# Performance work log

Measured on AMD Instinct MI355X. Metric: run time of the kernel, lower is better.

## Reference

```python
import jax, jax.numpy as jnp
import numpy as np

B, L, E, H = 2, 2048, 1024, 16
HD = E // H


def _rel_shift(x):
    # x: [b, h, q, k] -> Transformer-XL relative shift via pad+reshape trick
    b, h, q, k = x.shape
    xp = jnp.pad(x, ((0, 0), (0, 0), (0, 0), (1, 0)))  # pad left of last dim
    xp = xp.reshape(b, h, k + 1, q)
    return xp[:, :, 1:, :].reshape(b, h, q, k)


def setup_inputs() -> dict:
    key = jax.random.key(0)
    ks = jax.random.split(key, 16)
    s = 0.02
    return {
        "query": jax.random.normal(ks[0], (B, L, E), jnp.float32),
        "key": jax.random.normal(ks[1], (B, L, E), jnp.float32),
        "value": jax.random.normal(ks[2], (B, L, E), jnp.float32),
        "pos_embedding": jax.random.normal(ks[3], (B, L, E), jnp.float32),
        "Wq": jax.random.normal(ks[4], (E, E), jnp.float32) * s,
        "bq": jnp.zeros((E,), jnp.float32),
        "Wk": jax.random.normal(ks[5], (E, E), jnp.float32) * s,
        "bk": jnp.zeros((E,), jnp.float32),
        "Wv": jax.random.normal(ks[6], (E, E), jnp.float32) * s,
        "bv": jnp.zeros((E,), jnp.float32),
        "Wp": jax.random.normal(ks[7], (E, E), jnp.float32) * s,  # Pos linear, no bias
        "Wo": jax.random.normal(ks[8], (E, E), jnp.float32) * s,
        "bo": jnp.zeros((E,), jnp.float32),
        "U": jax.random.normal(ks[9], (H, HD), jnp.float32) * s,
        "V": jax.random.normal(ks[10], (H, HD), jnp.float32) * s,
    }


def reference(query, key, value, pos_embedding, Wq, bq, Wk, bk, Wv, bv, Wp, Wo, bo, U, V):
    b, qlen, e = query.shape
    h, hd = U.shape
    scale = jnp.sqrt(jnp.asarray(e, query.dtype))
    # torch Linear: y = x @ W.T + b
    q = (query @ Wq.T + bq).reshape(b, qlen, h, hd)
    k = (key @ Wk.T + bk).reshape(b, key.shape[1], h, hd)
    v = (value @ Wv.T + bv).reshape(b, value.shape[1], h, hd)
    r = (pos_embedding @ Wp.T).reshape(b, -1, h, hd)
    content_score = jnp.einsum("bqhd,bkhd->bhqk", q + U, k)
    position_score = jnp.einsum("bqhd,bkhd->bhqk", q + V, r)
    position_score = _rel_shift(position_score)
    attention_score = (content_score + position_score) / scale
    # NOTE: the original module applies NO softmax; faithful reproduction.
    # einsum 'bhqk,bvhd->bqhd' sums over both k (scores) and v (values).
    alpha = jnp.einsum("bhqk,bvhd->bqhd", attention_score, v).reshape(b, qlen, e)
    return alpha @ Wo.T + bo
```

## Files before the change

kernel.cpp:

```cpp
#include <hip/hip_runtime.h>

#define BB 2
#define LL 2048
#define EE 1024
#define HH 16
#define HDD 64

typedef __bf16 bf16x8 __attribute__((ext_vector_type(8)));
typedef float f32x4 __attribute__((ext_vector_type(4)));

__device__ __forceinline__ unsigned short f2bf(float f) {
  unsigned int x = __float_as_uint(f);
  return (unsigned short)((x + 0x7FFFu + ((x >> 16) & 1u)) >> 16);
}

__device__ __forceinline__ void load_lds16(const void* g, void* l) {
  __builtin_amdgcn_global_load_lds(
      (const __attribute__((address_space(1))) void*)g,
      (__attribute__((address_space(3))) void*)l, 16, 0, 0);
}

#define CAST_BLOCKS 1280
#define CAST_STRIDE (CAST_BLOCKS * 256)
__global__ __launch_bounds__(256) void prelude_kernel(
    const float* __restrict__ q, const float* __restrict__ pe,
    const float* __restrict__ wq, const float* __restrict__ wp,
    unsigned short* __restrict__ q16, unsigned short* __restrict__ pe16,
    unsigned short* __restrict__ wq16, unsigned short* __restrict__ wp16,
    const float* __restrict__ key, const float* __restrict__ value,
    float* __restrict__ keysum, float* __restrict__ valsum) {
  if (blockIdx.x < CAST_BLOCKS) {
    const int NQ4 = BB * LL * EE / 4;
    const int NW4 = EE * EE / 4;
    int t = blockIdx.x * 256 + threadIdx.x;
    float4 v[8]; unsigned short* dst[8]; int off[8];
#pragma unroll
    for (int k = 0; k < 8; k++) {
      int i = t + k * CAST_STRIDE;
      const float* src;
      if (i < NQ4)                { src = q;  dst[k] = q16;  off[k] = i; }
      else if (i < 2 * NQ4)       { src = pe; dst[k] = pe16; off[k] = i - NQ4; }
      else if (i < 2 * NQ4 + NW4) { src = wq; dst[k] = wq16; off[k] = i - 2 * NQ4; }
      else                        { src = wp; dst[k] = wp16; off[k] = i - 2 * NQ4 - NW4; }
      v[k] = ((const float4*)src)[off[k]];
    }
#pragma unroll
    for (int k = 0; k < 8; k++) {
      ushort4 u;
      u.x = f2bf(v[k].x); u.y = f2bf(v[k].y); u.z = f2bf(v[k].z); u.w = f2bf(v[k].w);
      ((ushort4*)dst[k])[off[k]] = u;
    }
  } else {
    int blk2 = blockIdx.x - CAST_BLOCKS;
    int b = blk2 >> 6, ch = blk2 & 63;
    int tid = threadIdx.x;
    const float4* k4 = (const float4*)(key   + ((size_t)b * LL + ch * 32) * EE);
    const float4* v4 = (const float4*)(value + ((size_t)b * LL + ch * 32) * EE);
    float4 ak = make_float4(0.f, 0.f, 0.f, 0.f);
    float4 av = make_float4(0.f, 0.f, 0.f, 0.f);
#pragma unroll 4
    for (int i = 0; i < 32; i++) {
      float4 kk = k4[i * 256 + tid];
      float4 vv = v4[i * 256 + tid];
      ak.x += kk.x; ak.y += kk.y; ak.z += kk.z; ak.w += kk.w;
      av.x += vv.x; av.y += vv.y; av.z += vv.z; av.w += vv.w;
    }
    int e = tid * 4;
    atomicAdd(&keysum[b * EE + e + 0], ak.x);
    atomicAdd(&keysum[b * EE + e + 1], ak.y);
    atomicAdd(&keysum[b * EE + e + 2], ak.z);
    atomicAdd(&keysum[b * EE + e + 3], ak.w);
    atomicAdd(&valsum[b * EE + e + 0], av.x);
    atomicAdd(&valsum[b * EE + e + 1], av.y);
    atomicAdd(&valsum[b * EE + e + 2], av.z);
    atomicAdd(&valsum[b * EE + e + 3], av.w);
  }
}

__global__ __launch_bounds__(256) void proj_kernel(
    const float* __restrict__ keysum, const float* __restrict__ valsum,
    const float* __restrict__ Wk, const float* __restrict__ bk,
    const float* __restrict__ Wv, const float* __restrict__ bv,
    float* __restrict__ Kproj, float* __restrict__ Vproj) {
  int wv = threadIdx.x >> 6, lane = threadIdx.x & 63;
  int idx = blockIdx.x * 4 + wv;
  int b = idx >> 10, ep = idx & (EE - 1);
  const float* sum  = blockIdx.z ? valsum : keysum;
  const float* W    = blockIdx.z ? Wv : Wk;
  const float* bias = blockIdx.z ? bv : bk;
  float* outp       = blockIdx.z ? Vproj : Kproj;
  float acc = 0.f;
  for (int k = lane; k < EE; k += 64) acc += sum[b * EE + k] * W[ep * EE + k];
  for (int off = 32; off; off >>= 1) acc += __shfl_down(acc, off, 64);
  if (lane == 0) outp[b * EE + ep] = acc + (float)LL * bias[ep];
}

__global__ __launch_bounds__(256) void w2_kernel(
    const float* __restrict__ Vproj, const float* __restrict__ Wo,
    float* __restrict__ W2) {
  int wv = threadIdx.x >> 6, lane = threadIdx.x & 63;
  int idx = blockIdx.x * 4 + wv;
  int e = idx & (EE - 1);
  int h = (idx >> 10) & (HH - 1);
  int b = idx >> 14;
  float acc = Vproj[b * EE + h * HDD + lane] * Wo[(size_t)e * EE + h * HDD + lane];
  for (int off = 32; off; off >>= 1) acc += __shfl_down(acc, off, 64);
  if (lane == 0) W2[((size_t)b * HH + h) * EE + e] = acc;
}

__global__ __launch_bounds__(256) void gemm_kernel(
    const unsigned short* __restrict__ q16, const unsigned short* __restrict__ wq16,
    const float* __restrict__ bq, float* __restrict__ qout,
    const unsigned short* __restrict__ pe16, const unsigned short* __restrict__ wp16,
    float* __restrict__ rout, float* __restrict__ chunks) {
  const int K = EE, N = EE;
  const unsigned short* X; const unsigned short* W; const float* bias; float* Out;
  if (blockIdx.z == 0) { X = q16;  W = wq16; bias = bq;      Out = qout; }
  else                 { X = pe16; W = wp16; bias = nullptr; Out = rout; }

  __shared__ __align__(16) unsigned short As[128 * 32];
  __shared__ __align__(16) unsigned short Bs[128 * 32];

  const int tid = threadIdx.x;
  const int lane = tid & 63;
  const int wv = tid >> 6;
  const int wr = wv >> 1, wc = wv & 1;
  const int n0 = blockIdx.x * 128;
  const int m0 = blockIdx.y * 128;

  const int srow = wv * 16 + (lane >> 2);
  const int scol = (lane & 3) * 8;
  const unsigned short* gA = X + (size_t)(m0 + srow) * K + scol;
  const unsigned short* gB = W + (size_t)(n0 + srow) * K + scol;
  unsigned short* sA = As + wv * 512;
  unsigned short* sB = Bs + wv * 512;

  f32x4 acc[4][4];
#pragma unroll
  for (int i = 0; i < 4; i++)
#pragma unroll
    for (int j = 0; j < 4; j++) acc[i][j] = (f32x4)0.0f;

  const int arow = wr * 64 + (lane & 15);
  const int brow = wc * 64 + (lane & 15);
  const int koff = (lane >> 4) * 8;

  for (int kk = 0; kk < K; kk += 32) {
    load_lds16(gA + kk,                   sA);
    load_lds16(gA + kk + (size_t)64 * K,  sA + 2048);
    load_lds16(gB + kk,                   sB);
    load_lds16(gB + kk + (size_t)64 * K,  sB + 2048);
    __syncthreads();
    bf16x8 af[4], bf[4];
#pragma unroll
    for (int i = 0; i < 4; i++) af[i] = *(const bf16x8*)&As[(arow + i * 16) * 32 + koff];
#pragma unroll
    for (int j = 0; j < 4; j++) bf[j] = *(const bf16x8*)&Bs[(brow + j * 16) * 32 + koff];
#pragma unroll
    for (int i = 0; i < 4; i++)
#pragma unroll
      for (int j = 0; j < 4; j++)
        acc[i][j] = __builtin_amdgcn_mfma_f32_16x16x32_bf16(af[i], bf[j], acc[i][j], 0, 0, 0);
    __syncthreads();
  }

  const int rbase = m0 + wr * 64 + (lane >> 4) * 4;
  const int cbase = n0 + wc * 64 + (lane & 15);
#pragma unroll
  for (int i = 0; i < 4; i++) {
#pragma unroll
    for (int j = 0; j < 4; j++) {
      int col = cbase + j * 16;
      float badd = bias ? bias[col] : 0.f;
#pragma unroll
      for (int g = 0; g < 4; g++) {
        int row = rbase + i * 16 + g;
        Out[(size_t)row * N + col] = acc[i][j][g] + badd;
      }
    }
  }

  if (blockIdx.z == 1) {
    int b = m0 >> 11;
    int ch0 = ((m0 & (LL - 1)) >> 5) + wr * 2;
#pragma unroll
    for (int cp = 0; cp < 2; cp++) {
#pragma unroll
      for (int j = 0; j < 4; j++) {
        float s = 0.f;
#pragma unroll
        for (int i = cp * 2; i < cp * 2 + 2; i++)
#pragma unroll
          for (int g = 0; g < 4; g++) s += acc[i][j][g];
        s += __shfl_down(s, 32, 64);
        s += __shfl_down(s, 16, 64);
        if (lane < 16) {
          int col = n0 + wc * 64 + j * 16 + lane;
          chunks[((size_t)b * 64 + ch0 + cp) * EE + col] = s;
        }
      }
    }
  }
}

__global__ __launch_bounds__(256) void scan2f_kernel(
    const float* __restrict__ qbuf, const float* __restrict__ rbuf,
    const float* __restrict__ chunks, const float* __restrict__ Kproj,
    const float* __restrict__ U, const float* __restrict__ V,
    float* __restrict__ S1, float* __restrict__ Dbuf) {
  int tid = threadIdx.x, lane = tid & 63;
  int hg = blockIdx.x, ch = blockIdx.y, b = blockIdx.z;
  int e = hg * 256 + tid;
  int h = hg * 4 + (tid >> 6);
  float pre = 0.f, tot = 0.f;
  for (int c = 0; c < 64; c++) {
    float cs = chunks[((size_t)b * 64 + c) * EE + e];
    tot += cs;
    if (c < ch) pre += cs;
  }
  float kp = Kproj[b * EE + e], Ue = U[e], Ve = V[e];
  float run = pre;
  size_t hoff = ((size_t)b * HH + h) * LL;
#pragma unroll 4
  for (int i = 0; i < 32; i++) {
    int m = ch * 32 + i;
    int p = LL - 1 - m;
    float qv = qbuf[((size_t)b * LL + p) * EE + e];
    float rv = rbuf[((size_t)b * LL + m) * EE + e];
    float tq = qv + Ve;
    float d = tq * run;
    float s = tq * tot + (qv + Ue) * kp;
#pragma unroll
    for (int off = 32; off; off >>= 1) {
      d += __shfl_down(d, off, 64);
      s += __shfl_down(s, off, 64);
    }
    if (lane == 0) { Dbuf[hoff + m] = d; S1[hoff + p] = s; }
    run += rv;
  }
}

__global__ __launch_bounds__(256) void out_kernel(
    const float* __restrict__ S1, const float* __restrict__ Dbuf,
    const float* __restrict__ W2, const float* __restrict__ bo,
    float* __restrict__ out) {
  int row = blockIdx.x;
  int b = row >> 11, p = row & (LL - 1);
  __shared__ float sh[HH];
  if (threadIdx.x < HH) {
    int h = threadIdx.x;
    size_t hoff = ((size_t)b * HH + h) * LL;
    float s1 = S1[hoff + p];
    float d1 = Dbuf[hoff + (LL - 1 - p)];
    float d2 = (p == LL - 1) ? 0.f : Dbuf[hoff + (LL - 2 - p)];
    sh[h] = (s1 - d1 + d2) * (1.f / 32.f);
  }
  __syncthreads();
  int e4 = threadIdx.x;
  const float4* W2v = (const float4*)W2;
  float4 acc = ((const float4*)bo)[e4];
#pragma unroll
  for (int h = 0; h < HH; h++) {
    float s = sh[h];
    float4 w = W2v[((size_t)b * HH + h) * 256 + e4];
    acc.x += s * w.x; acc.y += s * w.y; acc.z += s * w.z; acc.w += s * w.w;
  }
  ((float4*)out)[(size_t)row * 256 + e4] = acc;
}

extern "C" void kernel_launch(void* const* d_in, const int* in_sizes, int n_in,
                              void* d_out, int out_size, void* d_ws, size_t ws_size,
                              hipStream_t stream) {
  const float* query = (const float*)d_in[0];
  const float* key   = (const float*)d_in[1];
  const float* value = (const float*)d_in[2];
  const float* pos   = (const float*)d_in[3];
  const float* Wq = (const float*)d_in[4];
  const float* bq = (const float*)d_in[5];
  const float* Wk = (const float*)d_in[6];
  const float* bk = (const float*)d_in[7];
  const float* Wv = (const float*)d_in[8];
  const float* bv = (const float*)d_in[9];
  const float* Wp = (const float*)d_in[10];
  const float* Wo = (const float*)d_in[11];
  const float* bo = (const float*)d_in[12];
  const float* U  = (const float*)d_in[13];
  const float* V  = (const float*)d_in[14];
  float* out = (float*)d_out;

  char* ws = (char*)d_ws;
  size_t o = 0;
  auto take = [&](size_t bytes) -> char* {
    char* p = ws + o;
    o += (bytes + 255) & ~(size_t)255;
    return p;
  };
  float* keysum = (float*)take(BB * EE * 4);
  float* valsum = (float*)take(BB * EE * 4);
  float* Kproj  = (float*)take(BB * EE * 4);
  float* Vproj  = (float*)take(BB * EE * 4);
  float* W2     = (float*)take((size_t)BB * HH * EE * 4);
  float* S1     = (float*)take((size_t)BB * HH * LL * 4);
  float* Dbuf   = (float*)take((size_t)BB * HH * LL * 4);
  float* chunks = (float*)take((size_t)BB * 64 * EE * 4);
  float* qbuf   = (float*)take((size_t)BB * LL * EE * 4);
  float* rbuf   = (float*)take((size_t)BB * LL * EE * 4);
  unsigned short* q16  = (unsigned short*)take((size_t)BB * LL * EE * 2);
  unsigned short* pe16 = (unsigned short*)take((size_t)BB * LL * EE * 2);
  unsigned short* wq16 = (unsigned short*)take((size_t)EE * EE * 2);
  unsigned short* wp16 = (unsigned short*)take((size_t)EE * EE * 2);

  hipMemsetAsync(keysum, 0, (size_t)2 * BB * EE * 4, stream);

  prelude_kernel<<<CAST_BLOCKS + 128, 256, 0, stream>>>(
      query, pos, Wq, Wp, q16, pe16, wq16, wp16, key, value, keysum, valsum);
  proj_kernel<<<dim3(BB * EE / 4, 1, 2), 256, 0, stream>>>(keysum, valsum, Wk, bk, Wv, bv, Kproj, Vproj);
  w2_kernel<<<dim3(BB * HH * EE / 4), 256, 0, stream>>>(Vproj, Wo, W2);
  gemm_kernel<<<dim3(EE / 128, BB * LL / 128, 2), 256, 0, stream>>>(
      q16, wq16, bq, qbuf, pe16, wp16, rbuf, chunks);
  scan2f_kernel<<<dim3(4, 64, BB), 256, 0, stream>>>(qbuf, rbuf, chunks, Kproj, U, V, S1, Dbuf);
  out_kernel<<<dim3(BB * LL), 256, 0, stream>>>(S1, Dbuf, W2, bo, out);
}
```

Baseline: 230.0 us.

## Store projected q/r as bf16 and merge small projection kernels

The GEMM now writes the projected query and position tensors as bf16 instead of fp32, and the scan kernel widens them back on load. This halves the intermediate write and read traffic. The key/value projection and the Wo-folding kernels are merged into one 40-block launch, removing a launch and the Vproj buffer. The key/value sum blocks move to the front of the prelude with smaller chunks. This adds bf16 rounding error to q and r, and the merged small kernel has far fewer blocks, so it may become latency bound.

```diff
diff --git a/kernel.cpp b/kernel.cpp
--- a/kernel.cpp
+++ b/kernel.cpp
@@ -14,12 +14,17 @@
   return (unsigned short)((x + 0x7FFFu + ((x >> 16) & 1u)) >> 16);
 }
 
+__device__ __forceinline__ float bf2f(unsigned short u) {
+  return __uint_as_float((unsigned int)u << 16);
+}
+
 __device__ __forceinline__ void load_lds16(const void* g, void* l) {
   __builtin_amdgcn_global_load_lds(
       (const __attribute__((address_space(1))) void*)g,
       (__attribute__((address_space(3))) void*)l, 16, 0, 0);
 }
 
+#define SUMKV_BLOCKS 256
 #define CAST_BLOCKS 1280
 #define CAST_STRIDE (CAST_BLOCKS * 256)
 __global__ __launch_bounds__(256) void prelude_kernel(
@@ -29,37 +34,16 @@
     unsigned short* __restrict__ wq16, unsigned short* __restrict__ wp16,
     const float* __restrict__ key, const float* __restrict__ value,
     float* __restrict__ keysum, float* __restrict__ valsum) {
-  if (blockIdx.x < CAST_BLOCKS) {
-    const int NQ4 = BB * LL * EE / 4;
-    const int NW4 = EE * EE / 4;
-    int t = blockIdx.x * 256 + threadIdx.x;
-    float4 v[8]; unsigned short* dst[8]; int off[8];
-#pragma unroll
-    for (int k = 0; k < 8; k++) {
-      int i = t + k * CAST_STRIDE;
-      const float* src;
-      if (i < NQ4)                { src = q;  dst[k] = q16;  off[k] = i; }
-      else if (i < 2 * NQ4)       { src = pe; dst[k] = pe16; off[k] = i - NQ4; }
-      else if (i < 2 * NQ4 + NW4) { src = wq; dst[k] = wq16; off[k] = i - 2 * NQ4; }
-      else                        { src = wp; dst[k] = wp16; off[k] = i - 2 * NQ4 - NW4; }
-      v[k] = ((const float4*)src)[off[k]];
-    }
-#pragma unroll
-    for (int k = 0; k < 8; k++) {
-      ushort4 u;
-      u.x = f2bf(v[k].x); u.y = f2bf(v[k].y); u.z = f2bf(v[k].z); u.w = f2bf(v[k].w);
-      ((ushort4*)dst[k])[off[k]] = u;
-    }
-  } else {
-    int blk2 = blockIdx.x - CAST_BLOCKS;
-    int b = blk2 >> 6, ch = blk2 & 63;
+  if (blockIdx.x < SUMKV_BLOCKS) {
+    int blk2 = blockIdx.x;
+    int b = blk2 >> 7, ch = blk2 & 127;
     int tid = threadIdx.x;
-    const float4* k4 = (const float4*)(key   + ((size_t)b * LL + ch * 32) * EE);
-    const float4* v4 = (const float4*)(value + ((size_t)b * LL + ch * 32) * EE);
+    const float4* k4 = (const float4*)(key   + ((size_t)b * LL + ch * 16) * EE);
+    const float4* v4 = (const float4*)(value + ((size_t)b * LL + ch * 16) * EE);
     float4 ak = make_float4(0.f, 0.f, 0.f, 0.f);
     float4 av = make_float4(0.f, 0.f, 0.f, 0.f);
-#pragma unroll 4
-    for (int i = 0; i < 32; i++) {
+#pragma unroll 8
+    for (int i = 0; i < 16; i++) {
       float4 kk = k4[i * 256 + tid];
       float4 vv = v4[i * 256 + tid];
       ak.x += kk.x; ak.y += kk.y; ak.z += kk.z; ak.w += kk.w;
@@ -74,47 +58,88 @@
     atomicAdd(&valsum[b * EE + e + 1], av.y);
     atomicAdd(&valsum[b * EE + e + 2], av.z);
     atomicAdd(&valsum[b * EE + e + 3], av.w);
-  }
-}
-
-__global__ __launch_bounds__(256) void proj_kernel(
+  } else {
+    const int NQ4 = BB * LL * EE / 4;
+    const int NW4 = EE * EE / 4;
+    int t = (blockIdx.x - SUMKV_BLOCKS) * 256 + threadIdx.x;
+    float4 v[8]; unsigned short* dst[8]; int off[8];
+#pragma unroll
+    for (int k = 0; k < 8; k++) {
+      int i = t + k * CAST_STRIDE;
+      const float* src;
+      if (i < NQ4)                { src = q;  dst[k] = q16;  off[k] = i; }
+      else if (i < 2 * NQ4)       { src = pe; dst[k] = pe16; off[k] = i - NQ4; }
+      else if (i < 2 * NQ4 + NW4) { src = wq; dst[k] = wq16; off[k] = i - 2 * NQ4; }
+      else                        { src = wp; dst[k] = wp16; off[k] = i - 2 * NQ4 - NW4; }
+      v[k] = ((const float4*)src)[off[k]];
+    }
+#pragma unroll
+    for (int k = 0; k < 8; k++) {
+      ushort4 u;
+      u.x = f2bf(v[k].x); u.y = f2bf(v[k].y); u.z = f2bf(v[k].z); u.w = f2bf(v[k].w);
+      ((ushort4*)dst[k])[off[k]] = u;
+    }
+  }
+}
+
+__global__ __launch_bounds__(256) void small_kernel(
     const float* __restrict__ keysum, const float* __restrict__ valsum,
     const float* __restrict__ Wk, const float* __restrict__ bk,
     const float* __restrict__ Wv, const float* __restrict__ bv,
-    float* __restrict__ Kproj, float* __restrict__ Vproj) {
+    const float* __restrict__ Wo, float* __restrict__ Kproj,
+    float* __restrict__ W2) {
+  __shared__ float vsh[HDD];
   int wv = threadIdx.x >> 6, lane = threadIdx.x & 63;
-  int idx = blockIdx.x * 4 + wv;
-  int b = idx >> 10, ep = idx & (EE - 1);
-  const float* sum  = blockIdx.z ? valsum : keysum;
-  const float* W    = blockIdx.z ? Wv : Wk;
-  const float* bias = blockIdx.z ? bv : bk;
-  float* outp       = blockIdx.z ? Vproj : Kproj;
-  float acc = 0.f;
-  for (int k = lane; k < EE; k += 64) acc += sum[b * EE + k] * W[ep * EE + k];
-  for (int off = 32; off; off >>= 1) acc += __shfl_down(acc, off, 64);
-  if (lane == 0) outp[b * EE + ep] = acc + (float)LL * bias[ep];
-}
-
-__global__ __launch_bounds__(256) void w2_kernel(
-    const float* __restrict__ Vproj, const float* __restrict__ Wo,
-    float* __restrict__ W2) {
-  int wv = threadIdx.x >> 6, lane = threadIdx.x & 63;
-  int idx = blockIdx.x * 4 + wv;
-  int e = idx & (EE - 1);
-  int h = (idx >> 10) & (HH - 1);
-  int b = idx >> 14;
-  float acc = Vproj[b * EE + h * HDD + lane] * Wo[(size_t)e * EE + h * HDD + lane];
-  for (int off = 32; off; off >>= 1) acc += __shfl_down(acc, off, 64);
-  if (lane == 0) W2[((size_t)b * HH + h) * EE + e] = acc;
+  int blk = blockIdx.x;
+  if (blk < 32) {
+    int b = blk >> 4, h = blk & 15;
+    for (int dd = 0; dd < 16; dd++) {
+      int d = wv * 16 + dd;
+      int row = h * HDD + d;
+      float acc = 0.f;
+      for (int k = lane; k < EE; k += 64)
+        acc += valsum[b * EE + k] * Wv[(size_t)row * EE + k];
+      for (int off = 32; off; off >>= 1) acc += __shfl_down(acc, off, 64);
+      if (lane == 0) vsh[d] = acc + (float)LL * bv[row];
+    }
+    __syncthreads();
+    float4 vs[16];
+#pragma unroll
+    for (int i = 0; i < 16; i++) vs[i] = ((const float4*)vsh)[i];
+#pragma unroll
+    for (int j = 0; j < 4; j++) {
+      int e = threadIdx.x * 4 + j;
+      const float4* wo = (const float4*)(Wo + (size_t)e * EE + h * HDD);
+      float acc = 0.f;
+#pragma unroll
+      for (int i = 0; i < 16; i++) {
+        float4 w = wo[i];
+        acc += vs[i].x * w.x + vs[i].y * w.y + vs[i].z * w.z + vs[i].w * w.w;
+      }
+      W2[((size_t)b * HH + h) * EE + e] = acc;
+    }
+  } else {
+    int wslot = (blk - 32) * 4 + wv;
+    for (int r = 0; r < 64; r++) {
+      int idx = wslot * 64 + r;
+      int b = idx >> 10, ep = idx & (EE - 1);
+      float acc = 0.f;
+      for (int k = lane; k < EE; k += 64)
+        acc += keysum[b * EE + k] * Wk[(size_t)ep * EE + k];
+      for (int off = 32; off; off >>= 1) acc += __shfl_down(acc, off, 64);
+      if (lane == 0) Kproj[b * EE + ep] = acc + (float)LL * bk[ep];
+    }
+  }
 }
 
 __global__ __launch_bounds__(256) void gemm_kernel(
     const unsigned short* __restrict__ q16, const unsigned short* __restrict__ wq16,
-    const float* __restrict__ bq, float* __restrict__ qout,
+    const float* __restrict__ bq, unsigned short* __restrict__ qout,
     const unsigned short* __restrict__ pe16, const unsigned short* __restrict__ wp16,
-    float* __restrict__ rout, float* __restrict__ chunks) {
+    unsigned short* __restrict__ rout, float* __restrict__ chunks) {
   const int K = EE, N = EE;
-  const unsigned short* X; const unsigned short* W; const float* bias; float* Out;
+  const unsigned short* X; const unsigned short* W; const float* bias;
+  unsigned short* Out;
   if (blockIdx.z == 0) { X = q16;  W = wq16; bias = bq;      Out = qout; }
   else                 { X = pe16; W = wp16; bias = nullptr; Out = rout; }
 
@@ -175,7 +200,7 @@
 #pragma unroll
       for (int g = 0; g < 4; g++) {
         int row = rbase + i * 16 + g;
-        Out[(size_t)row * N + col] = acc[i][j][g] + badd;
+        Out[(size_t)row * N + col] = f2bf(acc[i][j][g] + badd);
       }
     }
   }
@@ -204,7 +229,7 @@
 }
 
 __global__ __launch_bounds__(256) void scan2f_kernel(
-    const float* __restrict__ qbuf, const float* __restrict__ rbuf,
+    const unsigned short* __restrict__ qbuf, const unsigned short* __restrict__ rbuf,
     const float* __restrict__ chunks, const float* __restrict__ Kproj,
     const float* __restrict__ U, const float* __restrict__ V,
     float* __restrict__ S1, float* __restrict__ Dbuf) {
@@ -225,8 +250,8 @@
   for (int i = 0; i < 32; i++) {
     int m = ch * 32 + i;
     int p = LL - 1 - m;
-    float qv = qbuf[((size_t)b * LL + p) * EE + e];
-    float rv = rbuf[((size_t)b * LL + m) * EE + e];
+    float qv = bf2f(qbuf[((size_t)b * LL + p) * EE + e]);
+    float rv = bf2f(rbuf[((size_t)b * LL + m) * EE + e]);
     float tq = qv + Ve;
     float d = tq * run;
     float s = tq * tot + (qv + Ue) * kp;
@@ -298,13 +323,12 @@
   float* keysum = (float*)take(BB * EE * 4);
   float* valsum = (float*)take(BB * EE * 4);
   float* Kproj  = (float*)take(BB * EE * 4);
-  float* Vproj  = (float*)take(BB * EE * 4);
   float* W2     = (float*)take((size_t)BB * HH * EE * 4);
   float* S1     = (float*)take((size_t)BB * HH * LL * 4);
   float* Dbuf   = (float*)take((size_t)BB * HH * LL * 4);
   float* chunks = (float*)take((size_t)BB * 64 * EE * 4);
-  float* qbuf   = (float*)take((size_t)BB * LL * EE * 4);
-  float* rbuf   = (float*)take((size_t)BB * LL * EE * 4);
+  unsigned short* qbuf = (unsigned short*)take((size_t)BB * LL * EE * 2);
+  unsigned short* rbuf = (unsigned short*)take((size_t)BB * LL * EE * 2);
   unsigned short* q16  = (unsigned short*)take((size_t)BB * LL * EE * 2);
   unsigned short* pe16 = (unsigned short*)take((size_t)BB * LL * EE * 2);
   unsigned short* wq16 = (unsigned short*)take((size_t)EE * EE * 2);
@@ -312,10 +336,9 @@
 
   hipMemsetAsync(keysum, 0, (size_t)2 * BB * EE * 4, stream);
 
-  prelude_kernel<<<CAST_BLOCKS + 128, 256, 0, stream>>>(
+  prelude_kernel<<<SUMKV_BLOCKS + CAST_BLOCKS, 256, 0, stream>>>(
       query, pos, Wq, Wp, q16, pe16, wq16, wp16, key, value, keysum, valsum);
-  proj_kernel<<<dim3(BB * EE / 4, 1, 2), 256, 0, stream>>>(keysum, valsum, Wk, bk, Wv, bv, Kproj, Vproj);
-  w2_kernel<<<dim3(BB * HH * EE / 4), 256, 0, stream>>>(Vproj, Wo, W2);
+  small_kernel<<<40, 256, 0, stream>>>(keysum, valsum, Wk, bk, Wv, bv, Wo, Kproj, W2);
   gemm_kernel<<<dim3(EE / 128, BB * LL / 128, 2), 256, 0, stream>>>(
       q16, wq16, bq, qbuf, pe16, wp16, rbuf, chunks);
   scan2f_kernel<<<dim3(4, 64, BB), 256, 0, stream>>>(qbuf, rbuf, chunks, Kproj, U, V, S1, Dbuf);
```

Measured after the change: 606.0 us. 2.63x slower.
